# Kernel tuning notes

Measured on AMD Instinct MI355X. Metric: run time of the kernel, lower is better.

## Reference

```python
import jax, jax.numpy as jnp
import numpy as np

B, L, C, H, W = 2, 4, 64, 80, 80
DISCRETE_RATIO, DOWNSAMPLE_RATE, NUM_ITER = 0.4, 2, 2


def _conv2d(x, w, b):
    y = jax.lax.conv_general_dilated(x, w, (1, 1), 'SAME',
                                     dimension_numbers=('NCHW', 'OIHW', 'NCHW'))
    return y + b[None, :, None, None]


def _get_transformation_matrix(M, h, w):
    # shift(center) @ [R 0; 0 1] @ shift(-center), then add raw translation (kornia-style)
    R = M[:, :2, :2]
    center = jnp.array([w / 2.0, h / 2.0], M.dtype)
    trans = center[None, :] - jnp.einsum('nij,j->ni', R, center) + M[:, :, 2]
    return jnp.concatenate([R, trans[:, :, None]], axis=2)  # (N,2,3)


def _warp_affine(src, M, mode):
    # src (N,C,h,w); M (N,2,3) maps src pixels -> dst pixels; sample src at M^{-1} @ dst
    # (equivalent to F.affine_grid/grid_sample with align_corners=True, zeros padding)
    N, Cc, h, w = src.shape
    bottom = jnp.tile(jnp.array([[[0.0, 0.0, 1.0]]], src.dtype), (N, 1, 1))
    Minv = jnp.linalg.inv(jnp.concatenate([M, bottom], axis=1))
    yy, xx = jnp.meshgrid(jnp.arange(h, dtype=src.dtype),
                          jnp.arange(w, dtype=src.dtype), indexing='ij')
    pts = jnp.stack([xx.ravel(), yy.ravel(), jnp.ones(h * w, src.dtype)], 0)  # (3,P)
    sp = jnp.einsum('nij,jp->nip', Minv, pts)
    sx, sy = sp[:, 0], sp[:, 1]  # (N,P) source pixel coords
    flat = src.reshape(N, Cc, h * w)

    def gather(ix, iy):
        valid = ((ix >= 0) & (ix < w) & (iy >= 0) & (iy < h)).astype(src.dtype)
        idx = jnp.clip(iy, 0, h - 1) * w + jnp.clip(ix, 0, w - 1)
        vals = jnp.take_along_axis(flat, jnp.broadcast_to(idx[:, None, :], (N, Cc, h * w)), axis=2)
        return vals * valid[:, None, :]

    if mode == 'nearest':
        out = gather(jnp.round(sx).astype(jnp.int32), jnp.round(sy).astype(jnp.int32))
    else:
        x0 = jnp.floor(sx); y0 = jnp.floor(sy)
        fx = (sx - x0)[:, None, :]; fy = (sy - y0)[:, None, :]
        x0 = x0.astype(jnp.int32); y0 = y0.astype(jnp.int32)
        out = (gather(x0, y0) * (1 - fx) * (1 - fy)
               + gather(x0 + 1, y0) * fx * (1 - fy)
               + gather(x0, y0 + 1) * (1 - fx) * fy
               + gather(x0 + 1, y0 + 1) * fx * fy)
    return out.reshape(N, Cc, h, w)


def _forward(x, pairwise_t_matrix, msg_w, msg_b, gates_w, gates_b, can_w, can_b, mlp_w, mlp_b):
    feats = x.reshape(B, L, C, H, W)
    # rows [0,1], cols [0,1,3] of the 4x4 SE(3) matrices; discretize translation
    t = pairwise_t_matrix[..., :2, :][..., jnp.array([0, 1, 3])]  # (B,L,L,2,3)
    t = t.at[..., 2].set(t[..., 2] / (DISCRETE_RATIO * DOWNSAMPLE_RATE))
    T = _get_transformation_matrix(t.reshape(-1, 2, 3), H, W)  # (B*L*L,2,3), flat index (b, j, i)
    mask = _warp_affine(jnp.ones((B * L * L, 1, H, W), x.dtype), T, 'nearest').reshape(B, L, L, 1, H, W)

    for _ in range(NUM_ITER):
        # 'b c h w -> b c w h' + flip(last): coordinate-convention fix (H==W)
        y = jnp.flip(jnp.swapaxes(feats, -1, -2), axis=-1)  # (B,L,C,H,W)
        # warp neighbor j into ego i frame with T[b,j,i]
        src = jnp.broadcast_to(y[:, :, None], (B, L, L, C, H, W)).reshape(-1, C, H, W)
        neighbor = _warp_affine(src, T, 'bilinear')
        ego = jnp.broadcast_to(y[:, None], (B, L, L, C, H, W)).reshape(-1, C, H, W)
        msg = _conv2d(jnp.concatenate([neighbor, ego], axis=1), msg_w, msg_b)
        msg = msg.reshape(B, L, L, C, H, W) * mask
        agg = msg.mean(axis=1)  # 'avg' over neighbors j -> (B,L,C,H,W)
        cat_feat = jnp.concatenate([y, agg], axis=2).reshape(B * L, 2 * C, H, W)
        # single ConvGRU step with zero initial hidden state
        h0 = jnp.zeros((B * L, C, H, W), x.dtype)
        gates = _conv2d(jnp.concatenate([cat_feat, h0], axis=1), gates_w, gates_b)
        reset = jax.nn.sigmoid(gates[:, :C])
        update = jax.nn.sigmoid(gates[:, C:])
        cand = jnp.tanh(_conv2d(jnp.concatenate([cat_feat, reset * h0], axis=1), can_w, can_b))
        h1 = (1.0 - update) * h0 + update * cand
        # undo the coordinate fix: flip(last) then 'c w h -> c h w'
        feats = jnp.swapaxes(jnp.flip(h1.reshape(B, L, C, H, W), axis=-1), -1, -2)

    out = feats[:, 0]  # ego agent of each sample, (B,C,H,W)
    return jnp.einsum('bchw,oc->bhwo', out, mlp_w) + mlp_b  # nn.Linear on channel-last


def setup_inputs() -> dict:
    key = jax.random.key(0)
    ks = jax.random.split(key, 12)
    x = jax.random.normal(ks[0], (B * L, C, H, W), dtype=jnp.float32)
    record_len = jnp.full((B,), L, dtype=jnp.int32)
    # realistic SE(2) pairwise transforms embedded in 4x4 homogeneous matrices
    ang = jax.random.uniform(ks[1], (B, L, L), minval=-0.3, maxval=0.3)
    tx = jax.random.uniform(ks[2], (B, L, L), minval=-8.0, maxval=8.0)
    ty = jax.random.uniform(ks[3], (B, L, L), minval=-8.0, maxval=8.0)
    c, s = jnp.cos(ang), jnp.sin(ang)
    z, o = jnp.zeros_like(ang), jnp.ones_like(ang)
    pairwise_t_matrix = jnp.stack([c, -s, z, tx,
                                   s, c, z, ty,
                                   z, z, o, z,
                                   z, z, z, o], axis=-1).reshape(B, L, L, 4, 4).astype(jnp.float32)
    prior_encoding = jax.random.normal(ks[4], (B * L, 3), dtype=jnp.float32)  # unused by forward
    sc = 0.05
    return {
        'x': x,
        'record_len': record_len,
        'pairwise_t_matrix': pairwise_t_matrix,
        'prior_encoding': prior_encoding,
        'msg_w': jax.random.normal(ks[5], (C, 2 * C, 3, 3), dtype=jnp.float32) * sc,
        'msg_b': jnp.zeros((C,), jnp.float32),
        'gates_w': jax.random.normal(ks[6], (2 * C, 3 * C, 3, 3), dtype=jnp.float32) * sc,
        'gates_b': jnp.zeros((2 * C,), jnp.float32),
        'can_w': jax.random.normal(ks[7], (C, 3 * C, 3, 3), dtype=jnp.float32) * sc,
        'can_b': jnp.zeros((C,), jnp.float32),
        'mlp_w': jax.random.normal(ks[8], (C, C), dtype=jnp.float32) * sc,
        'mlp_b': jnp.zeros((C,), jnp.float32),
    }


def reference(x, record_len, pairwise_t_matrix, prior_encoding,
              msg_w, msg_b, gates_w, gates_b, can_w, can_b, mlp_w, mlp_b):
    # record_len is fixed to L for every sample; prior_encoding is unused by the torch forward
    return _forward(x, pairwise_t_matrix, msg_w, msg_b, gates_w, gates_b,
                    can_w, can_b, mlp_w, mlp_b)
```

## Files before the change

### kernel.cpp

```cpp
#include <hip/hip_runtime.h>
#include <math.h>

#define WD 80
#define HW 6400
#define PW 82
#define PPX 6790
#define NIMG 8
#define NPAIR 32
#define TSTG 960

typedef short bf16x8 __attribute__((ext_vector_type(8)));
typedef float f32x4 __attribute__((ext_vector_type(4)));

__device__ __forceinline__ float bf2f(unsigned short u) {
    return __uint_as_float(((unsigned)u) << 16);
}
__device__ __forceinline__ unsigned short f2bf(float f) {
    unsigned u = __float_as_uint(f);
    u += 0x7fff + ((u >> 16) & 1);
    return (unsigned short)(u >> 16);
}

__device__ __forceinline__ void inv_affine(const float* __restrict__ P, int p, float* a) {
    const float* m = P + p * 16;
    float m00 = m[0], m01 = m[1], m02 = m[3] / 0.8f;
    float m10 = m[4], m11 = m[5], m12 = m[7] / 0.8f;
    float cx = 40.0f, cy = 40.0f;
    float tx = cx - (m00 * cx + m01 * cy) + m02;
    float ty = cy - (m10 * cx + m11 * cy) + m12;
    float id = 1.0f / (m00 * m11 - m01 * m10);
    a[0] =  m11 * id; a[1] = -m01 * id;
    a[3] = -m10 * id; a[4] =  m00 * id;
    a[2] = -(a[0] * tx + a[1] * ty);
    a[5] = -(a[3] * tx + a[4] * ty);
}

__global__ void prologue(const float* __restrict__ P, float* __restrict__ mats,
                         float* __restrict__ mask,
                         const float* __restrict__ msg_w, const float* __restrict__ gates_w,
                         const float* __restrict__ can_w,
                         unsigned short* __restrict__ Wn, unsigned short* __restrict__ We,
                         unsigned short* __restrict__ Wu, unsigned short* __restrict__ Wc) {
    int bx = blockIdx.x;
    if (bx < 32) {
        int p = bx;
        float a[6];
        inv_affine(P, p, a);
        if (threadIdx.x < 6) mats[p * 6 + threadIdx.x] = a[threadIdx.x];
        for (int q = threadIdx.x; q < HW; q += blockDim.x) {
            float x = (float)(q % WD), y = (float)(q / WD);
            float sx = a[0] * x + a[1] * y + a[2];
            float sy = a[3] * x + a[4] * y + a[5];
            int ix = (int)rintf(sx), iy = (int)rintf(sy);
            mask[p * HW + q] = (ix >= 0 && ix < WD && iy >= 0 && iy < WD) ? 1.0f : 0.0f;
        }
        return;
    }
    int t = (bx - 32) * 256 + threadIdx.x;
    if (t >= 221184) return;
    const float* src; unsigned short* dst;
    int cin_n, co_off, ci_off, stride, u;
    if (t < 36864)       { src = msg_w;   dst = Wn; cin_n = 64;  co_off = 0;  ci_off = 0;  stride = 1152; u = t; }
    else if (t < 73728)  { src = msg_w;   dst = We; cin_n = 64;  co_off = 0;  ci_off = 64; stride = 1152; u = t - 36864; }
    else if (t < 147456) { src = gates_w; dst = Wu; cin_n = 128; co_off = 64; ci_off = 0;  stride = 1728; u = t - 73728; }
    else                 { src = can_w;   dst = Wc; cin_n = 128; co_off = 0;  ci_off = 0;  stride = 1728; u = t - 147456; }
    int ci = u % cin_n;
    int co = (u / cin_n) & 63;
    int tap = u / (cin_n * 64);
    dst[u] = f2bf(src[(size_t)(co_off + co) * stride + (ci_off + ci) * 9 + tap]);
}

__global__ void zero_borders(unsigned short* __restrict__ bufs) {
    int idx = blockIdx.x * blockDim.x + threadIdx.x;
    if (idx >= 24 * 324 * 8) return;
    int g = idx & 7;
    int e = (idx >> 3) % 324;
    int img = idx / (324 * 8);
    int pp;
    if (e < 82)       pp = e;
    else if (e < 164) pp = 81 * PW + (e - 82);
    else if (e < 244) pp = (e - 164 + 1) * PW;
    else              pp = (e - 244 + 1) * PW + 81;
    *(uint4*)(bufs + ((size_t)img * PPX + pp) * 64 + g * 8) = (uint4){0, 0, 0, 0};
}

__global__ __launch_bounds__(256) void rot_init_t(const float* __restrict__ x,
                                                  unsigned short* __restrict__ Y) {
    __shared__ float T[64][81];
    int img = blockIdx.x / 80, hh = blockIdx.x % 80;
    int tid = threadIdx.x;
    for (int idx = tid; idx < 64 * 80; idx += 256) {
        int c = idx / 80, ww = idx % 80;
        T[c][ww] = x[((size_t)(img * 64 + c) * 80 + hh) * 80 + ww];
    }
    __syncthreads();
    int b = 79 - hh;
    for (int idx = tid; idx < 80 * 64; idx += 256) {
        int a = idx >> 6, ch = idx & 63;
        Y[((size_t)img * PPX + (a + 1) * PW + (b + 1)) * 64 + ch] = f2bf(T[ch][a]);
    }
}

__global__ void warp_pairs(const unsigned short* __restrict__ Ysrc, const float* __restrict__ mats,
                           unsigned short* __restrict__ warped, int total, int only0) {
    int idx = blockIdx.x * blockDim.x + threadIdx.x;
    if (idx >= total) return;
    int g = idx & 7;
    int pp = (idx >> 3) % 6724;
    int k = idx / (6724 * 8);
    int p = only0 ? k * 4 : k;
    int py = pp / PW, pxx = pp % PW;
    uint4 v = {0, 0, 0, 0};
    if (py >= 1 && py <= 80 && pxx >= 1 && pxx <= 80) {
        int y = py - 1, x = pxx - 1;
        const float* a = mats + p * 6;
        float sx = a[0] * x + a[1] * y + a[2];
        float sy = a[3] * x + a[4] * y + a[5];
        float fxf = floorf(sx), fyf = floorf(sy);
        float fx = sx - fxf, fy = sy - fyf;
        int ix = (int)fxf, iy = (int)fyf;
        float w00 = (1.f - fx) * (1.f - fy), w10 = fx * (1.f - fy);
        float w01 = (1.f - fx) * fy,         w11 = fx * fy;
        bool vx0 = (unsigned)ix < WD, vx1 = (unsigned)(ix + 1) < WD;
        bool vy0 = (unsigned)iy < WD, vy1 = (unsigned)(iy + 1) < WD;
        if (!(vx0 && vy0)) w00 = 0.f;
        if (!(vx1 && vy0)) w10 = 0.f;
        if (!(vx0 && vy1)) w01 = 0.f;
        if (!(vx1 && vy1)) w11 = 0.f;
        int cx0 = min(max(ix, 0), WD - 1), cx1 = min(max(ix + 1, 0), WD - 1);
        int cy0 = min(max(iy, 0), WD - 1), cy1 = min(max(iy + 1, 0), WD - 1);
        const unsigned short* src = Ysrc + (size_t)(p >> 2) * PPX * 64 + g * 8;
        uint4 c00 = *(const uint4*)(src + ((cy0 + 1) * PW + cx0 + 1) * 64);
        uint4 c10 = *(const uint4*)(src + ((cy0 + 1) * PW + cx1 + 1) * 64);
        uint4 c01 = *(const uint4*)(src + ((cy1 + 1) * PW + cx0 + 1) * 64);
        uint4 c11 = *(const uint4*)(src + ((cy1 + 1) * PW + cx1 + 1) * 64);
        const unsigned short* p00 = (const unsigned short*)&c00;
        const unsigned short* p10 = (const unsigned short*)&c10;
        const unsigned short* p01 = (const unsigned short*)&c01;
        const unsigned short* p11 = (const unsigned short*)&c11;
        unsigned short r8[8];
#pragma unroll
        for (int kk = 0; kk < 8; ++kk) {
            float vv = w00 * bf2f(p00[kk]) + w10 * bf2f(p10[kk])
                     + w01 * bf2f(p01[kk]) + w11 * bf2f(p11[kk]);
            r8[kk] = f2bf(vv);
        }
        v = *(const uint4*)r8;
    }
    *(uint4*)(warped + ((size_t)k * PPX + pp) * 64 + g * 8) = v;
}

__device__ __forceinline__ void stage_t(const unsigned short* __restrict__ src,
                                        int x0, int y0, uint4* bufbase, int tid) {
    const int lane = tid & 63;
    const int wv = tid >> 6;
    for (int c = wv; c < TSTG / 64; c += 4) {
        int s = c * 64 + lane;
        int q = s >> 3;
        int yl = q / 20, xl = q - yl * 20;
        int g = (s & 7) ^ (q & 7);
        const unsigned short* gp = src + ((y0 + yl) * PW + x0 + xl) * 64 + g * 8;
        __builtin_amdgcn_global_load_lds(
            (const __attribute__((address_space(1))) unsigned int*)gp,
            (__attribute__((address_space(3))) unsigned int*)(bufbase + c * 64),
            16, 0, 0);
    }
}

__device__ __forceinline__ void load_w(const unsigned short* __restrict__ W, int row,
                                       int cinstride, int cin0, int lh, bf16x8* Wf) {
#pragma unroll
    for (int ks = 0; ks < 2; ++ks)
#pragma unroll
        for (int tap = 0; tap < 9; ++tap)
            Wf[ks * 9 + tap] = *(const bf16x8*)(W + (size_t)(tap * 64 + row) * cinstride
                                                + cin0 + ks * 32 + lh * 8);
}

__device__ __forceinline__ void conv_pass4(const uint4* __restrict__ buf, const bf16x8* Wf,
                                           int ll, int lh, f32x4* acc) {
#pragma unroll
    for (int ks = 0; ks < 2; ++ks) {
        const int g = ks * 4 + lh;
#pragma unroll
        for (int tx = 0; tx < 3; ++tx) {
            bf16x8 A[6];
#pragma unroll
            for (int s = 0; s < 6; ++s) {
                int q = s * 20 + tx + ll;
                A[s] = *(const bf16x8*)&buf[q * 8 + (g ^ (q & 7))];
            }
#pragma unroll
            for (int ty = 0; ty < 3; ++ty) {
                bf16x8 B = Wf[ks * 9 + ty * 3 + tx];
#pragma unroll
                for (int r = 0; r < 4; ++r)
                    acc[r] = __builtin_amdgcn_mfma_f32_16x16x32_bf16(A[r + ty], B, acc[r], 0, 0, 0);
            }
        }
    }
}

__global__ __launch_bounds__(256, 2) void msg_agg(const unsigned short* __restrict__ warped,
        const unsigned short* __restrict__ Y, const float* __restrict__ mask,
        const unsigned short* __restrict__ Wn, const unsigned short* __restrict__ We,
        const float* __restrict__ bias, unsigned short* __restrict__ Gpad, int only0) {
    __shared__ uint4 lds[2 * TSTG];
    __shared__ float lmask[4][4][16];
    const int tid = threadIdx.x, lane = tid & 63, wv = tid >> 6;
    const int ll = lane & 15, lh = lane >> 4;
    const int x0 = blockIdx.x * 16, y0 = blockIdx.y * 4;
    const int t = blockIdx.z;
    const int b = only0 ? t : (t >> 2), j = only0 ? 0 : (t & 3);
    const int img = only0 ? t * 4 : t;
    const int row = wv * 16 + ll;

    int ks_[4];
#pragma unroll
    for (int i = 0; i < 4; ++i)
        ks_[i] = only0 ? (b * 4 + i) : ((b * 4 + i) * 4 + j);
    {
        int i = tid >> 6, r = (tid >> 4) & 3, px = tid & 15;
        int p = only0 ? ks_[i] * 4 : ks_[i];
        lmask[i][r][px] = mask[(size_t)p * HW + (y0 + r) * WD + x0 + px];
    }
    bf16x8 Wf[18];
    load_w(Wn, row, 64, 0, lh, Wf);
    stage_t(warped + (size_t)ks_[0] * PPX * 64, x0, y0, lds, tid);
    __syncthreads();

    f32x4 tot[4];
#pragma unroll
    for (int r = 0; r < 4; ++r) tot[r] = (f32x4){0.f, 0.f, 0.f, 0.f};

    for (int i = 0; i < 4; ++i) {
        if (i < 3)
            stage_t(warped + (size_t)ks_[i + 1] * PPX * 64, x0, y0, lds + ((i + 1) & 1) * TSTG, tid);
        else
            stage_t(Y + (size_t)img * PPX * 64, x0, y0, lds, tid);
        f32x4 acc[4];
#pragma unroll
        for (int r = 0; r < 4; ++r) acc[r] = (f32x4){0.f, 0.f, 0.f, 0.f};
        conv_pass4(lds + (i & 1) * TSTG, Wf, ll, lh, acc);
#pragma unroll
        for (int r = 0; r < 4; ++r)
#pragma unroll
            for (int jj = 0; jj < 4; ++jj)
                tot[r][jj] += lmask[i][r][lh * 4 + jj] * acc[r][jj];
        __syncthreads();
    }

    load_w(We, row, 64, 0, lh, Wf);
    f32x4 acc[4];
#pragma unroll
    for (int r = 0; r < 4; ++r) acc[r] = (f32x4){0.f, 0.f, 0.f, 0.f};
    conv_pass4(lds, Wf, ll, lh, acc);

    float bv = bias[row];
#pragma unroll
    for (int r = 0; r < 4; ++r)
#pragma unroll
        for (int jj = 0; jj < 4; ++jj) {
            int px = lh * 4 + jj;
            float msum = lmask[0][r][px] + lmask[1][r][px] + lmask[2][r][px] + lmask[3][r][px];
            float val = 0.25f * (tot[r][jj] + msum * (acc[r][jj] + bv));
            Gpad[((size_t)t * PPX + (y0 + r + 1) * PW + (x0 + px + 1)) * 64 + row] = f2bf(val);
        }
}

__global__ __launch_bounds__(256, 2) void gru_conv(const unsigned short* __restrict__ Ysrc,
        const unsigned short* __restrict__ Gpad,
        const unsigned short* __restrict__ Wu, const unsigned short* __restrict__ Wc,
        const float* __restrict__ bu, const float* __restrict__ bc,
        unsigned short* __restrict__ Ydst, int only0) {
    __shared__ uint4 lds[2 * TSTG];
    const int tid = threadIdx.x, lane = tid & 63, wv = tid >> 6;
    const int ll = lane & 15, lh = lane >> 4;
    const int x0 = blockIdx.x * 16, y0 = blockIdx.y * 4;
    const int t = blockIdx.z;
    const int img = only0 ? t * 4 : t;
    const int row = wv * 16 + ll;

    stage_t(Ysrc + (size_t)img * PPX * 64, x0, y0, lds, tid);
    stage_t(Gpad + (size_t)t * PPX * 64, x0, y0, lds + TSTG, tid);
    bf16x8 Wf[18];
    load_w(Wu, row, 128, 0, lh, Wf);
    __syncthreads();

    f32x4 aU[4], aC[4];
#pragma unroll
    for (int r = 0; r < 4; ++r) {
        aU[r] = (f32x4){0.f, 0.f, 0.f, 0.f};
        aC[r] = (f32x4){0.f, 0.f, 0.f, 0.f};
    }
    conv_pass4(lds, Wf, ll, lh, aU);
    load_w(Wu, row, 128, 64, lh, Wf);
    conv_pass4(lds + TSTG, Wf, ll, lh, aU);
    load_w(Wc, row, 128, 0, lh, Wf);
    conv_pass4(lds, Wf, ll, lh, aC);
    load_w(Wc, row, 128, 64, lh, Wf);
    conv_pass4(lds + TSTG, Wf, ll, lh, aC);

    float ub = bu[row], cb = bc[row];
#pragma unroll
    for (int r = 0; r < 4; ++r)
#pragma unroll
        for (int jj = 0; jj < 4; ++jj) {
            int x = x0 + lh * 4 + jj;
            float u = 1.f / (1.f + __expf(-(aU[r][jj] + ub)));
            float e2 = __expf(2.f * (aC[r][jj] + cb));
            float c = (e2 - 1.f) / (e2 + 1.f);
            Ydst[((size_t)img * PPX + (y0 + r + 1) * PW + (x + 1)) * 64 + row] = f2bf(u * c);
        }
}

__global__ void final_mlp(const unsigned short* __restrict__ yfin, const float* __restrict__ mw,
                          const float* __restrict__ mb, float* __restrict__ out) {
    int t = blockIdx.x * blockDim.x + threadIdx.x;
    if (t >= 2 * HW * 64) return;
    int o  = t & 63;
    int wv = (t >> 6) % WD;
    int h  = ((t >> 6) / WD) % WD;
    int b  = t / (HW * 64);
    const unsigned short* src = yfin + ((size_t)(b * 4) * PPX + (wv + 1) * PW + (80 - h)) * 64;
    const float* wrow = mw + o * 64;
    float r = mb[o];
#pragma unroll
    for (int c8 = 0; c8 < 8; ++c8) {
        bf16x8 v = *(const bf16x8*)(src + c8 * 8);
#pragma unroll
        for (int k = 0; k < 8; ++k)
            r += bf2f(((const unsigned short*)&v)[k]) * wrow[c8 * 8 + k];
    }
    out[t] = r;
}

extern "C" void kernel_launch(void* const* d_in, const int* in_sizes, int n_in,
                              void* d_out, int out_size, void* d_ws, size_t ws_size,
                              hipStream_t stream) {
    const float* x       = (const float*)d_in[0];
    const float* P       = (const float*)d_in[2];
    const float* msg_w   = (const float*)d_in[4];
    const float* msg_b   = (const float*)d_in[5];
    const float* gates_w = (const float*)d_in[6];
    const float* gates_b = (const float*)d_in[7];
    const float* can_w   = (const float*)d_in[8];
    const float* can_b   = (const float*)d_in[9];
    const float* mlp_w   = (const float*)d_in[10];
    const float* mlp_b   = (const float*)d_in[11];
    float* out = (float*)d_out;

    char* wsb = (char*)d_ws;
    float* mats = (float*)wsb;
    float* mask = (float*)(wsb + 1024);
    unsigned short* Wn = (unsigned short*)(wsb + 820224);
    unsigned short* We = Wn + 36864;
    unsigned short* Wu = We + 36864;
    unsigned short* Wc = Wu + 73728;
    unsigned short* Y0 = Wc + 73728;
    unsigned short* Y1 = Y0 + (size_t)NIMG * PPX * 64;
    unsigned short* Gpad = Y1 + (size_t)NIMG * PPX * 64;
    unsigned short* warped = Gpad + (size_t)NIMG * PPX * 64;

    zero_borders<<<(24 * 324 * 8 + 255) / 256, 256, 0, stream>>>(Y0);
    prologue<<<32 + (221184 + 255) / 256, 256, 0, stream>>>(P, mats, mask,
        msg_w, gates_w, can_w, Wn, We, Wu, Wc);
    rot_init_t<<<NIMG * 80, 256, 0, stream>>>(x, Y0);

    warp_pairs<<<(32 * 6724 * 8 + 255) / 256, 256, 0, stream>>>(Y0, mats, warped, 32 * 6724 * 8, 0);
    msg_agg<<<dim3(5, 20, 8), 256, 0, stream>>>(warped, Y0, mask, Wn, We, msg_b, Gpad, 0);
    gru_conv<<<dim3(5, 20, 8), 256, 0, stream>>>(Y0, Gpad, Wu, Wc, gates_b + 64, can_b, Y1, 0);

    warp_pairs<<<(8 * 6724 * 8 + 255) / 256, 256, 0, stream>>>(Y1, mats, warped, 8 * 6724 * 8, 1);
    msg_agg<<<dim3(5, 20, 2), 256, 0, stream>>>(warped, Y1, mask, Wn, We, msg_b, Gpad, 1);
    gru_conv<<<dim3(5, 20, 2), 256, 0, stream>>>(Y1, Gpad, Wu, Wc, gates_b + 64, can_b, Y0, 1);

    final_mlp<<<(2 * HW * 64 + 255) / 256, 256, 0, stream>>>(Y0, mlp_w, mlp_b, out);
}
```

Baseline: 237.9 us.

## Fuse bilinear warp into message conv staging and merge prologue kernels

The separate warp_pairs kernels, which wrote warped neighbour features to a global buffer, are removed. msg_agg now computes the bilinear warp on the fly while staging each neighbour tile into LDS. The zero_borders, prologue and rot_init_t kernels are also merged into one launch to cut launch count. This drops a full global write and re-read of the warped tensors plus several launches. In exchange, the staging path now does synchronous gathers and arithmetic instead of async global_load_lds, recomputes halo pixels per tile, and the merged kernel reserves static LDS even in blocks that never use it.

```diff
diff --git a/kernel.cpp b/kernel.cpp
--- a/kernel.cpp
+++ b/kernel.cpp
@@ -35,59 +35,62 @@
     a[5] = -(a[3] * tx + a[4] * ty);
 }
 
-__global__ void prologue(const float* __restrict__ P, float* __restrict__ mats,
-                         float* __restrict__ mask,
-                         const float* __restrict__ msg_w, const float* __restrict__ gates_w,
-                         const float* __restrict__ can_w,
-                         unsigned short* __restrict__ Wn, unsigned short* __restrict__ We,
-                         unsigned short* __restrict__ Wu, unsigned short* __restrict__ Wc) {
+__global__ __launch_bounds__(256) void prologue_all(
+        const float* __restrict__ P, float* __restrict__ mats, float* __restrict__ mask,
+        const float* __restrict__ msg_w, const float* __restrict__ gates_w,
+        const float* __restrict__ can_w,
+        unsigned short* __restrict__ Wn, unsigned short* __restrict__ We,
+        unsigned short* __restrict__ Wu, unsigned short* __restrict__ Wc,
+        const float* __restrict__ x, unsigned short* __restrict__ bufs) {
+    __shared__ float T[64][81];
     int bx = blockIdx.x;
+    if (bx < 243) {
+        int idx = bx * 256 + threadIdx.x;
+        if (idx >= 24 * 324 * 8) return;
+        int g = idx & 7;
+        int e = (idx >> 3) % 324;
+        int img = idx / (324 * 8);
+        int pp;
+        if (e < 82)       pp = e;
+        else if (e < 164) pp = 81 * PW + (e - 82);
+        else if (e < 244) pp = (e - 164 + 1) * PW;
+        else              pp = (e - 244 + 1) * PW + 81;
+        *(uint4*)(bufs + ((size_t)img * PPX + pp) * 64 + g * 8) = (uint4){0, 0, 0, 0};
+        return;
+    }
+    bx -= 243;
     if (bx < 32) {
         int p = bx;
         float a[6];
         inv_affine(P, p, a);
         if (threadIdx.x < 6) mats[p * 6 + threadIdx.x] = a[threadIdx.x];
         for (int q = threadIdx.x; q < HW; q += blockDim.x) {
-            float x = (float)(q % WD), y = (float)(q / WD);
-            float sx = a[0] * x + a[1] * y + a[2];
-            float sy = a[3] * x + a[4] * y + a[5];
+            float xx = (float)(q % WD), yy = (float)(q / WD);
+            float sx = a[0] * xx + a[1] * yy + a[2];
+            float sy = a[3] * xx + a[4] * yy + a[5];
             int ix = (int)rintf(sx), iy = (int)rintf(sy);
             mask[p * HW + q] = (ix >= 0 && ix < WD && iy >= 0 && iy < WD) ? 1.0f : 0.0f;
         }
         return;
     }
-    int t = (bx - 32) * 256 + threadIdx.x;
-    if (t >= 221184) return;
-    const float* src; unsigned short* dst;
-    int cin_n, co_off, ci_off, stride, u;
-    if (t < 36864)       { src = msg_w;   dst = Wn; cin_n = 64;  co_off = 0;  ci_off = 0;  stride = 1152; u = t; }
-    else if (t < 73728)  { src = msg_w;   dst = We; cin_n = 64;  co_off = 0;  ci_off = 64; stride = 1152; u = t - 36864; }
-    else if (t < 147456) { src = gates_w; dst = Wu; cin_n = 128; co_off = 64; ci_off = 0;  stride = 1728; u = t - 73728; }
-    else                 { src = can_w;   dst = Wc; cin_n = 128; co_off = 0;  ci_off = 0;  stride = 1728; u = t - 147456; }
-    int ci = u % cin_n;
-    int co = (u / cin_n) & 63;
-    int tap = u / (cin_n * 64);
-    dst[u] = f2bf(src[(size_t)(co_off + co) * stride + (ci_off + ci) * 9 + tap]);
-}
-
-__global__ void zero_borders(unsigned short* __restrict__ bufs) {
-    int idx = blockIdx.x * blockDim.x + threadIdx.x;
-    if (idx >= 24 * 324 * 8) return;
-    int g = idx & 7;
-    int e = (idx >> 3) % 324;
-    int img = idx / (324 * 8);
-    int pp;
-    if (e < 82)       pp = e;
-    else if (e < 164) pp = 81 * PW + (e - 82);
-    else if (e < 244) pp = (e - 164 + 1) * PW;
-    else              pp = (e - 244 + 1) * PW + 81;
-    *(uint4*)(bufs + ((size_t)img * PPX + pp) * 64 + g * 8) = (uint4){0, 0, 0, 0};
-}
-
-__global__ __launch_bounds__(256) void rot_init_t(const float* __restrict__ x,
-                                                  unsigned short* __restrict__ Y) {
-    __shared__ float T[64][81];
-    int img = blockIdx.x / 80, hh = blockIdx.x % 80;
+    bx -= 32;
+    if (bx < 864) {
+        int t = bx * 256 + threadIdx.x;
+        if (t >= 221184) return;
+        const float* src; unsigned short* dst;
+        int cin_n, co_off, ci_off, stride, u;
+        if (t < 36864)       { src = msg_w;   dst = Wn; cin_n = 64;  co_off = 0;  ci_off = 0;  stride = 1152; u = t; }
+        else if (t < 73728)  { src = msg_w;   dst = We; cin_n = 64;  co_off = 0;  ci_off = 64; stride = 1152; u = t - 36864; }
+        else if (t < 147456) { src = gates_w; dst = Wu; cin_n = 128; co_off = 64; ci_off = 0;  stride = 1728; u = t - 73728; }
+        else                 { src = can_w;   dst = Wc; cin_n = 128; co_off = 0;  ci_off = 0;  stride = 1728; u = t - 147456; }
+        int ci = u % cin_n;
+        int co = (u / cin_n) & 63;
+        int tap = u / (cin_n * 64);
+        dst[u] = f2bf(src[(size_t)(co_off + co) * stride + (ci_off + ci) * 9 + tap]);
+        return;
+    }
+    bx -= 864;
+    int img = bx / 80, hh = bx % 80;
     int tid = threadIdx.x;
     for (int idx = tid; idx < 64 * 80; idx += 256) {
         int c = idx / 80, ww = idx % 80;
@@ -97,57 +100,8 @@
     int b = 79 - hh;
     for (int idx = tid; idx < 80 * 64; idx += 256) {
         int a = idx >> 6, ch = idx & 63;
-        Y[((size_t)img * PPX + (a + 1) * PW + (b + 1)) * 64 + ch] = f2bf(T[ch][a]);
-    }
-}
-
-__global__ void warp_pairs(const unsigned short* __restrict__ Ysrc, const float* __restrict__ mats,
-                           unsigned short* __restrict__ warped, int total, int only0) {
-    int idx = blockIdx.x * blockDim.x + threadIdx.x;
-    if (idx >= total) return;
-    int g = idx & 7;
-    int pp = (idx >> 3) % 6724;
-    int k = idx / (6724 * 8);
-    int p = only0 ? k * 4 : k;
-    int py = pp / PW, pxx = pp % PW;
-    uint4 v = {0, 0, 0, 0};
-    if (py >= 1 && py <= 80 && pxx >= 1 && pxx <= 80) {
-        int y = py - 1, x = pxx - 1;
-        const float* a = mats + p * 6;
-        float sx = a[0] * x + a[1] * y + a[2];
-        float sy = a[3] * x + a[4] * y + a[5];
-        float fxf = floorf(sx), fyf = floorf(sy);
-        float fx = sx - fxf, fy = sy - fyf;
-        int ix = (int)fxf, iy = (int)fyf;
-        float w00 = (1.f - fx) * (1.f - fy), w10 = fx * (1.f - fy);
-        float w01 = (1.f - fx) * fy,         w11 = fx * fy;
-        bool vx0 = (unsigned)ix < WD, vx1 = (unsigned)(ix + 1) < WD;
-        bool vy0 = (unsigned)iy < WD, vy1 = (unsigned)(iy + 1) < WD;
-        if (!(vx0 && vy0)) w00 = 0.f;
-        if (!(vx1 && vy0)) w10 = 0.f;
-        if (!(vx0 && vy1)) w01 = 0.f;
-        if (!(vx1 && vy1)) w11 = 0.f;
-        int cx0 = min(max(ix, 0), WD - 1), cx1 = min(max(ix + 1, 0), WD - 1);
-        int cy0 = min(max(iy, 0), WD - 1), cy1 = min(max(iy + 1, 0), WD - 1);
-        const unsigned short* src = Ysrc + (size_t)(p >> 2) * PPX * 64 + g * 8;
-        uint4 c00 = *(const uint4*)(src + ((cy0 + 1) * PW + cx0 + 1) * 64);
-        uint4 c10 = *(const uint4*)(src + ((cy0 + 1) * PW + cx1 + 1) * 64);
-        uint4 c01 = *(const uint4*)(src + ((cy1 + 1) * PW + cx0 + 1) * 64);
-        uint4 c11 = *(const uint4*)(src + ((cy1 + 1) * PW + cx1 + 1) * 64);
-        const unsigned short* p00 = (const unsigned short*)&c00;
-        const unsigned short* p10 = (const unsigned short*)&c10;
-        const unsigned short* p01 = (const unsigned short*)&c01;
-        const unsigned short* p11 = (const unsigned short*)&c11;
-        unsigned short r8[8];
-#pragma unroll
-        for (int kk = 0; kk < 8; ++kk) {
-            float vv = w00 * bf2f(p00[kk]) + w10 * bf2f(p10[kk])
-                     + w01 * bf2f(p01[kk]) + w11 * bf2f(p11[kk]);
-            r8[kk] = f2bf(vv);
-        }
-        v = *(const uint4*)r8;
-    }
-    *(uint4*)(warped + ((size_t)k * PPX + pp) * 64 + g * 8) = v;
+        bufs[((size_t)img * PPX + (a + 1) * PW + (b + 1)) * 64 + ch] = f2bf(T[ch][a]);
+    }
 }
 
 __device__ __forceinline__ void stage_t(const unsigned short* __restrict__ src,
@@ -167,6 +121,52 @@
     }
 }
 
+__device__ __forceinline__ void stage_warp(const unsigned short* __restrict__ src,
+        const float* __restrict__ am, int x0, int y0, uint4* bufbase, int tid) {
+    float a0 = am[0], a1 = am[1], a2 = am[2], a3 = am[3], a4 = am[4], a5 = am[5];
+    for (int idx = tid; idx < TSTG; idx += 256) {
+        int q = idx >> 3, g = idx & 7;
+        int yl = q / 20, xl = q - yl * 20;
+        int ux = x0 + xl - 1, uy = y0 + yl - 1;
+        uint4 v = {0, 0, 0, 0};
+        if ((unsigned)ux < WD && (unsigned)uy < WD) {
+            float sx = a0 * ux + a1 * uy + a2;
+            float sy = a3 * ux + a4 * uy + a5;
+            float fxf = floorf(sx), fyf = floorf(sy);
+            float fx = sx - fxf, fy = sy - fyf;
+            int ix = (int)fxf, iy = (int)fyf;
+            float w00 = (1.f - fx) * (1.f - fy), w10 = fx * (1.f - fy);
+            float w01 = (1.f - fx) * fy,         w11 = fx * fy;
+            bool vx0 = (unsigned)ix < WD, vx1 = (unsigned)(ix + 1) < WD;
+            bool vy0 = (unsigned)iy < WD, vy1 = (unsigned)(iy + 1) < WD;
+            if (!(vx0 && vy0)) w00 = 0.f;
+            if (!(vx1 && vy0)) w10 = 0.f;
+            if (!(vx0 && vy1)) w01 = 0.f;
+            if (!(vx1 && vy1)) w11 = 0.f;
+            int cx0 = min(max(ix, 0), WD - 1), cx1 = min(max(ix + 1, 0), WD - 1);
+            int cy0 = min(max(iy, 0), WD - 1), cy1 = min(max(iy + 1, 0), WD - 1);
+            const unsigned short* s8 = src + g * 8;
+            uint4 c00 = *(const uint4*)(s8 + ((cy0 + 1) * PW + cx0 + 1) * 64);
+            uint4 c10 = *(const uint4*)(s8 + ((cy0 + 1) * PW + cx1 + 1) * 64);
+            uint4 c01 = *(const uint4*)(s8 + ((cy1 + 1) * PW + cx0 + 1) * 64);
+            uint4 c11 = *(const uint4*)(s8 + ((cy1 + 1) * PW + cx1 + 1) * 64);
+            const unsigned short* p00 = (const unsigned short*)&c00;
+            const unsigned short* p10 = (const unsigned short*)&c10;
+            const unsigned short* p01 = (const unsigned short*)&c01;
+            const unsigned short* p11 = (const unsigned short*)&c11;
+            unsigned short r8[8];
+#pragma unroll
+            for (int kk = 0; kk < 8; ++kk) {
+                float vv = w00 * bf2f(p00[kk]) + w10 * bf2f(p10[kk])
+                         + w01 * bf2f(p01[kk]) + w11 * bf2f(p11[kk]);
+                r8[kk] = f2bf(vv);
+            }
+            v = *(const uint4*)r8;
+        }
+        bufbase[q * 8 + (g ^ (q & 7))] = v;
+    }
+}
+
 __device__ __forceinline__ void load_w(const unsigned short* __restrict__ W, int row,
                                        int cinstride, int cin0, int lh, bf16x8* Wf) {
 #pragma unroll
@@ -201,8 +201,8 @@
     }
 }
 
-__global__ __launch_bounds__(256, 2) void msg_agg(const unsigned short* __restrict__ warped,
-        const unsigned short* __restrict__ Y, const float* __restrict__ mask,
+__global__ __launch_bounds__(256, 2) void msg_agg(const unsigned short* __restrict__ Y,
+        const float* __restrict__ mats, const float* __restrict__ mask,
         const unsigned short* __restrict__ Wn, const unsigned short* __restrict__ We,
         const float* __restrict__ bias, unsigned short* __restrict__ Gpad, int only0) {
     __shared__ uint4 lds[2 * TSTG];
@@ -215,18 +215,19 @@
     const int img = only0 ? t * 4 : t;
     const int row = wv * 16 + ll;
 
-    int ks_[4];
-#pragma unroll
-    for (int i = 0; i < 4; ++i)
-        ks_[i] = only0 ? (b * 4 + i) : ((b * 4 + i) * 4 + j);
+    int ps_[4];
+#pragma unroll
+    for (int i = 0; i < 4; ++i) {
+        int k = only0 ? (b * 4 + i) : ((b * 4 + i) * 4 + j);
+        ps_[i] = only0 ? k * 4 : k;
+    }
     {
         int i = tid >> 6, r = (tid >> 4) & 3, px = tid & 15;
-        int p = only0 ? ks_[i] * 4 : ks_[i];
-        lmask[i][r][px] = mask[(size_t)p * HW + (y0 + r) * WD + x0 + px];
+        lmask[i][r][px] = mask[(size_t)ps_[i] * HW + (y0 + r) * WD + x0 + px];
     }
     bf16x8 Wf[18];
     load_w(Wn, row, 64, 0, lh, Wf);
-    stage_t(warped + (size_t)ks_[0] * PPX * 64, x0, y0, lds, tid);
+    stage_warp(Y + (size_t)(b * 4 + 0) * PPX * 64, mats + ps_[0] * 6, x0, y0, lds, tid);
     __syncthreads();
 
     f32x4 tot[4];
@@ -235,7 +236,8 @@
 
     for (int i = 0; i < 4; ++i) {
         if (i < 3)
-            stage_t(warped + (size_t)ks_[i + 1] * PPX * 64, x0, y0, lds + ((i + 1) & 1) * TSTG, tid);
+            stage_warp(Y + (size_t)(b * 4 + i + 1) * PPX * 64, mats + ps_[i + 1] * 6,
+                       x0, y0, lds + ((i + 1) & 1) * TSTG, tid);
         else
             stage_t(Y + (size_t)img * PPX * 64, x0, y0, lds, tid);
         f32x4 acc[4];
@@ -360,19 +362,14 @@
     unsigned short* Y0 = Wc + 73728;
     unsigned short* Y1 = Y0 + (size_t)NIMG * PPX * 64;
     unsigned short* Gpad = Y1 + (size_t)NIMG * PPX * 64;
-    unsigned short* warped = Gpad + (size_t)NIMG * PPX * 64;
-
-    zero_borders<<<(24 * 324 * 8 + 255) / 256, 256, 0, stream>>>(Y0);
-    prologue<<<32 + (221184 + 255) / 256, 256, 0, stream>>>(P, mats, mask,
-        msg_w, gates_w, can_w, Wn, We, Wu, Wc);
-    rot_init_t<<<NIMG * 80, 256, 0, stream>>>(x, Y0);
-
-    warp_pairs<<<(32 * 6724 * 8 + 255) / 256, 256, 0, stream>>>(Y0, mats, warped, 32 * 6724 * 8, 0);
-    msg_agg<<<dim3(5, 20, 8), 256, 0, stream>>>(warped, Y0, mask, Wn, We, msg_b, Gpad, 0);
+
+    prologue_all<<<243 + 32 + 864 + 640, 256, 0, stream>>>(P, mats, mask,
+        msg_w, gates_w, can_w, Wn, We, Wu, Wc, x, Y0);
+
+    msg_agg<<<dim3(5, 20, 8), 256, 0, stream>>>(Y0, mats, mask, Wn, We, msg_b, Gpad, 0);
     gru_conv<<<dim3(5, 20, 8), 256, 0, stream>>>(Y0, Gpad, Wu, Wc, gates_b + 64, can_b, Y1, 0);
 
-    warp_pairs<<<(8 * 6724 * 8 + 255) / 256, 256, 0, stream>>>(Y1, mats, warped, 8 * 6724 * 8, 1);
-    msg_agg<<<dim3(5, 20, 2), 256, 0, stream>>>(warped, Y1, mask, Wn, We, msg_b, Gpad, 1);
+    msg_agg<<<dim3(5, 20, 2), 256, 0, stream>>>(Y1, mats, mask, Wn, We, msg_b, Gpad, 1);
     gru_conv<<<dim3(5, 20, 2), 256, 0, stream>>>(Y1, Gpad, Wu, Wc, gates_b + 64, can_b, Y0, 1);
 
     final_mlp<<<(2 * HW * 64 + 255) / 256, 256, 0, stream>>>(Y0, mlp_w, mlp_b, out);
```

Measured after the change: 239.5 us. No clear change (+0.7%).
